# Kernel optimization log

Measured on AMD Instinct MI355X. Metric: run time of the kernel, lower is better.

The kernel has to match this reference:

```python
import jax, jax.numpy as jnp
import numpy as np

H = 768
NH = 12
HD = H // NH

def _layernorm(x, g, b, eps=1e-5):
    mu = jnp.mean(x, axis=-1, keepdims=True)
    var = jnp.var(x, axis=-1, keepdims=True)
    return (x - mu) * jax.lax.rsqrt(var + eps) * g + b

def setup_inputs() -> dict:
    key = jax.random.key(0)
    ks = jax.random.split(key, 16)
    s = 0.02
    inp = {
        "x": jax.random.normal(ks[0], (2, 2048, H), jnp.float32),
        "t": jax.random.normal(ks[1], (2, 1, H), jnp.float32),
        # MHA params
        "w_qkv": jax.random.normal(ks[2], (H, 3 * H), jnp.float32) * s,
        "b_qkv": jnp.zeros((3 * H,), jnp.float32),
        "w_mffn1": jax.random.normal(ks[3], (H, 4 * H), jnp.float32) * s,
        "b_mffn1": jnp.zeros((4 * H,), jnp.float32),
        "w_mffn2": jax.random.normal(ks[4], (4 * H, H), jnp.float32) * s,
        "b_mffn2": jnp.zeros((H,), jnp.float32),
        # scale_shift (adaLN) params
        "w_ss1": jax.random.normal(ks[5], (H, 6 * H), jnp.float32) * s,
        "b_ss1": jnp.zeros((6 * H,), jnp.float32),
        "w_ss2": jax.random.normal(ks[6], (6 * H, 6 * H), jnp.float32) * s,
        "b_ss2": jnp.zeros((6 * H,), jnp.float32),
        # layernorms
        "ln1_g": jnp.ones((H,), jnp.float32),
        "ln1_b": jnp.zeros((H,), jnp.float32),
        "ln2_g": jnp.ones((H,), jnp.float32),
        "ln2_b": jnp.zeros((H,), jnp.float32),
        # DiT block FFN
        "w_ffn1": jax.random.normal(ks[7], (H, 4 * H), jnp.float32) * s,
        "b_ffn1": jnp.zeros((4 * H,), jnp.float32),
        "w_ffn2": jax.random.normal(ks[8], (4 * H, H), jnp.float32) * s,
        "b_ffn2": jnp.zeros((H,), jnp.float32),
    }
    return inp

def _mha(x, w_qkv, b_qkv, w1, b1, w2, b2):
    B, T, _ = x.shape
    qkv = x @ w_qkv + b_qkv                      # [B,T,3H]
    qkv = qkv.reshape(B, T, 3, NH, HD)           # split (n h s) as in rearrange
    q, k, v = [jnp.transpose(qkv[:, :, i], (0, 2, 1, 3)) for i in range(3)]  # [B,NH,T,HD]
    # NOTE: faithful to source: scale by 1/sqrt(hidden_size), not head_dim
    wei = jnp.einsum('bhtd,bhsd->bhts', q, k) / jnp.sqrt(jnp.asarray(H, x.dtype))
    wei = jax.nn.softmax(wei, axis=-1)           # [B,NH,T,T] (dropout p=0)
    o = jnp.einsum('bhts,bhsd->bhtd', wei, v)    # [B,NH,T,HD]
    o = jnp.transpose(o, (0, 2, 1, 3)).reshape(B, T, H)
    o = jax.nn.gelu(o @ w1 + b1, approximate=False) @ w2 + b2
    return o

def reference(x, t, w_qkv, b_qkv, w_mffn1, b_mffn1, w_mffn2, b_mffn2,
              w_ss1, b_ss1, w_ss2, b_ss2, ln1_g, ln1_b, ln2_g, ln2_b,
              w_ffn1, b_ffn1, w_ffn2, b_ffn2):
    t_emb = jax.nn.silu(t @ w_ss1 + b_ss1) @ w_ss2 + b_ss2   # [B,1,6H]
    g1, be1, a1, g2, be2, a2 = jnp.split(t_emb, 6, axis=-1)  # each [B,1,H]
    residual = x
    h = g1 * _layernorm(x, ln1_g, ln1_b) + be1
    h = _mha(h, w_qkv, b_qkv, w_mffn1, b_mffn1, w_mffn2, b_mffn2)
    x = residual + a1 * h
    residual = x
    h = g2 * _layernorm(x, ln2_g, ln2_b) + be2
    h = jax.nn.gelu(h @ w_ffn1 + b_ffn1, approximate=False) @ w_ffn2 + b_ffn2
    x = residual + a2 * h
    return x
```

## Files before the change

### kernel.cpp

```cpp
#include <hip/hip_runtime.h>
#include <hip/hip_bf16.h>
#include <cstdint>

typedef __bf16 bf16x8 __attribute__((ext_vector_type(8)));
typedef float f32x4 __attribute__((ext_vector_type(4)));

#define SCALE_Q_LOG2E 0.052058770734702875f

__device__ inline float fast_exp2(float x) { return __builtin_amdgcn_exp2f(x); }

struct TransAll {
  const float* src[5];
  __hip_bfloat16* dst[5];
  int K[5], N[5];
  int start[6];
};

__global__ void k_transpose_all(TransAll ta) {
  __shared__ float tile[32][33];
  int bid = blockIdx.x;
  int i = 0;
#pragma unroll
  for (int j = 1; j < 5; ++j)
    if (bid >= ta.start[j]) i = j;
  int t0 = bid - ta.start[i];
  int N = ta.N[i], K = ta.K[i];
  int ntx = N >> 5;
  int bx = t0 % ntx, by = t0 / ntx;
  const float* src = ta.src[i];
  __hip_bfloat16* dst = ta.dst[i];
  int n0 = bx * 32, k0 = by * 32;
  int tx = threadIdx.x & 31, ty = threadIdx.x >> 5;
#pragma unroll
  for (int r = 0; r < 32; r += 8)
    tile[ty + r][tx] = src[(size_t)(k0 + ty + r) * N + n0 + tx];
  __syncthreads();
#pragma unroll
  for (int r = 0; r < 32; r += 8)
    dst[(size_t)(n0 + ty + r) * K + k0 + tx] = __float2bfloat16(tile[tx][ty + r]);
}

__global__ void k_tvec_gemm(const float* __restrict__ tin, const float* __restrict__ W,
                            float* __restrict__ acc_out, int K, int N, int KC) {
  int n = blockIdx.x * 256 + threadIdx.x;
  int kb = blockIdx.y * KC;
  float a0 = 0.f, a1 = 0.f;
  for (int k = kb; k < kb + KC; ++k) {
    float w = W[(size_t)k * N + n];
    a0 += tin[k] * w;
    a1 += tin[K + k] * w;
  }
  atomicAdd(&acc_out[n], a0);
  atomicAdd(&acc_out[N + n], a1);
}

__global__ void k_silu_bias(const float* __restrict__ acc, const float* __restrict__ bias,
                            float* __restrict__ out) {
  int i = blockIdx.x * 256 + threadIdx.x;
  int n = i; if (n >= 4608) n -= 4608;
  float v = acc[i] + bias[n];
  out[i] = v / (1.f + expf(-v));
}

__global__ void k_bias_add(const float* __restrict__ acc, const float* __restrict__ bias,
                           float* __restrict__ out) {
  int i = blockIdx.x * 256 + threadIdx.x;
  int n = i; if (n >= 4608) n -= 4608;
  out[i] = acc[i] + bias[n];
}

__global__ void k_ln_mod(const float* __restrict__ x, const float* __restrict__ lng,
                         const float* __restrict__ lnb, const float* __restrict__ temb,
                         int gofs, int bofs, __hip_bfloat16* __restrict__ out) {
  int row = blockIdx.x;
  int b = row >> 11;
  const float* xr = x + (size_t)row * 768;
  int tid = threadIdx.x;
  float v[3];
  float s = 0.f, sq = 0.f;
#pragma unroll
  for (int i = 0; i < 3; ++i) { v[i] = xr[tid + 256 * i]; s += v[i]; sq += v[i] * v[i]; }
#pragma unroll
  for (int o = 32; o > 0; o >>= 1) { s += __shfl_xor(s, o); sq += __shfl_xor(sq, o); }
  __shared__ float rs[4], rq[4];
  int w = tid >> 6, lane = tid & 63;
  if (lane == 0) { rs[w] = s; rq[w] = sq; }
  __syncthreads();
  s = rs[0] + rs[1] + rs[2] + rs[3];
  sq = rq[0] + rq[1] + rq[2] + rq[3];
  float mu = s * (1.f / 768.f);
  float var = sq * (1.f / 768.f) - mu * mu;
  float rstd = rsqrtf(var + 1e-5f);
  const float* tb = temb + (size_t)b * 4608;
#pragma unroll
  for (int i = 0; i < 3; ++i) {
    int n = tid + 256 * i;
    float h = (v[i] - mu) * rstd * lng[n] + lnb[n];
    h = tb[gofs + n] * h + tb[bofs + n];
    out[(size_t)row * 768 + n] = __float2bfloat16(h);
  }
}

template <int BM, int BN, int EPI>
__global__ __launch_bounds__(256)
void k_gemm(const __hip_bfloat16* __restrict__ A,
            const __hip_bfloat16* __restrict__ Bt,
            const float* __restrict__ bias,
            float* __restrict__ outF, __hip_bfloat16* __restrict__ outB,
            const float* __restrict__ res, const float* __restrict__ temb,
            int gofs, int M, int N, int K) {
  constexpr int MI = BM / 32;
  constexpr int NI = BN / 32;
  __shared__ __align__(16) __hip_bfloat16 As[BM * 64];
  __shared__ __align__(16) __hip_bfloat16 Bs[BN * 64];
  const int tid = threadIdx.x;
  const int w = tid >> 6, lane = tid & 63;
  const int quad = lane >> 4, l16 = lane & 15;
  const int wm = w & 1, wn = w >> 1;
  const int m0 = blockIdx.y * BM, n0 = blockIdx.x * BN;
  const int srow = lane >> 3;
  const int sco = ((lane & 7) ^ srow) * 8;

  f32x4 acc[MI][NI] = {};

  for (int k0 = 0; k0 < K; k0 += 64) {
#pragma unroll
    for (int ii = 0; ii < BM / 32; ++ii) {
      int is = w * (BM / 32) + ii;
      const __hip_bfloat16* g = A + (size_t)(m0 + is * 8 + srow) * K + k0 + sco;
      __builtin_amdgcn_global_load_lds(
          (const __attribute__((address_space(1))) void*)g,
          (__attribute__((address_space(3))) void*)&As[is * 512], 16, 0, 0);
    }
#pragma unroll
    for (int ii = 0; ii < BN / 32; ++ii) {
      int is = w * (BN / 32) + ii;
      const __hip_bfloat16* g = Bt + (size_t)(n0 + is * 8 + srow) * K + k0 + sco;
      __builtin_amdgcn_global_load_lds(
          (const __attribute__((address_space(1))) void*)g,
          (__attribute__((address_space(3))) void*)&Bs[is * 512], 16, 0, 0);
    }
    __syncthreads();
#pragma unroll
    for (int ks = 0; ks < 2; ++ks) {
      bf16x8 af[MI], bfv[NI];
#pragma unroll
      for (int i = 0; i < MI; ++i) {
        int row = wm * (BM / 2) + i * 16 + l16;
        int cph = (ks * 4 + quad) ^ (row & 7);
        af[i] = *(const bf16x8*)&As[row * 64 + cph * 8];
      }
#pragma unroll
      for (int j = 0; j < NI; ++j) {
        int row = wn * (BN / 2) + j * 16 + l16;
        int cph = (ks * 4 + quad) ^ (row & 7);
        bfv[j] = *(const bf16x8*)&Bs[row * 64 + cph * 8];
      }
#pragma unroll
      for (int i = 0; i < MI; ++i)
#pragma unroll
        for (int j = 0; j < NI; ++j)
          acc[i][j] = __builtin_amdgcn_mfma_f32_16x16x32_bf16(af[i], bfv[j], acc[i][j], 0, 0, 0);
    }
    __syncthreads();
  }

#pragma unroll
  for (int j = 0; j < NI; ++j) {
    int col = n0 + wn * (BN / 2) + j * 16 + l16;
    float bs = bias[col];
#pragma unroll
    for (int i = 0; i < MI; ++i) {
#pragma unroll
      for (int r = 0; r < 4; ++r) {
        int row = m0 + wm * (BM / 2) + i * 16 + quad * 4 + r;
        float v = acc[i][j][r] + bs;
        size_t idx = (size_t)row * N + col;
        if (EPI == 0) {
          outF[idx] = v;
        } else if (EPI == 1) {
          float v2 = v * v;
          float u = v * (0.79788456080286536f + 0.035677408136300125f * v2);
          float e = fast_exp2(u * 2.8853900817779268f);
          float gl = v - v * __builtin_amdgcn_rcpf(e + 1.f);
          outB[idx] = __float2bfloat16(gl);
        } else if (EPI == 2) {
          float gate = temb[(size_t)(row >> 11) * 4608 + gofs + col];
          outF[idx] = res[idx] + gate * v;
        } else {
          float vq = (col < 768) ? v * SCALE_Q_LOG2E : v;
          outB[idx] = __float2bfloat16(vq);
        }
      }
    }
  }
}

__global__ void k_prep_vt(const __hip_bfloat16* __restrict__ qkvb,
                          __hip_bfloat16* __restrict__ VT) {
  __shared__ float Vs[64][65];
  int st = blockIdx.x, bh = blockIdx.y;
  int b = bh / 12, nh = bh - b * 12;
  int tid = threadIdx.x;
  {
    int r = tid & 63, c0 = (tid >> 6) * 16;
    const __hip_bfloat16* src =
        qkvb + (size_t)(b * 2048 + st * 64 + r) * 2304 + 1536 + nh * 64 + c0;
    uint4 raw0 = *(const uint4*)src;
    uint4 raw1 = *(const uint4*)(src + 8);
    const __hip_bfloat16* e0 = (const __hip_bfloat16*)&raw0;
    const __hip_bfloat16* e1 = (const __hip_bfloat16*)&raw1;
#pragma unroll
    for (int j = 0; j < 8; ++j) Vs[r][c0 + j] = __bfloat162float(e0[j]);
#pragma unroll
    for (int j = 0; j < 8; ++j) Vs[r][c0 + 8 + j] = __bfloat162float(e1[j]);
  }
  __syncthreads();
  {
    int d = tid >> 2, s0 = (tid & 3) * 16;
    __hip_bfloat16 tmp[16];
#pragma unroll
    for (int j = 0; j < 16; ++j) tmp[j] = __float2bfloat16(Vs[s0 + j][d]);
    __hip_bfloat16* dst = VT + (size_t)(bh * 64 + d) * 2048 + st * 64 + s0;
    *(uint4*)dst = *(uint4*)&tmp[0];
    *(uint4*)(dst + 8) = *(uint4*)&tmp[8];
  }
}

__launch_bounds__(256)
__global__ void k_attn(const __hip_bfloat16* __restrict__ qkvb,
                       const __hip_bfloat16* __restrict__ VT,
                       __hip_bfloat16* __restrict__ out) {
  __shared__ __align__(16) __hip_bfloat16 Ks[128 * 64];
  __shared__ __align__(16) __hip_bfloat16 Vs[64 * 128];
  __shared__ __align__(16) __hip_bfloat16 Pw[4][16 * 128];

  const int tid = threadIdx.x;
  const int w = tid >> 6, lane = tid & 63;
  const int quad = lane >> 4, l16 = lane & 15;
  const int qt = blockIdx.x, nh = blockIdx.y, b = blockIdx.z;
  const int bh = b * 12 + nh;

  const int qrow0 = b * 2048 + qt * 64 + w * 16;
  bf16x8 qf[2];
#pragma unroll
  for (int t = 0; t < 2; ++t)
    qf[t] = *(const bf16x8*)(qkvb + (size_t)(qrow0 + l16) * 2304 + nh * 64 + t * 32 + quad * 8);

  bf16x8 ones;
#pragma unroll
  for (int j = 0; j < 8; ++j) ones[j] = (__bf16)1.0f;

  f32x4 o[4] = {};
  f32x4 o_l = {};

  const int srow8 = lane >> 3;
  const int sco8 = ((lane & 7) ^ srow8) * 8;
  const int srow4 = lane >> 4;

  for (int kt = 0; kt < 16; ++kt) {
    __syncthreads();
#pragma unroll
    for (int ii = 0; ii < 4; ++ii) {
      int i = w * 4 + ii;
      const __hip_bfloat16* gk =
          qkvb + (size_t)(b * 2048 + kt * 128 + i * 8 + srow8) * 2304 + 768 + nh * 64 + sco8;
      __builtin_amdgcn_global_load_lds(
          (const __attribute__((address_space(1))) void*)gk,
          (__attribute__((address_space(3))) void*)&Ks[i * 512], 16, 0, 0);
      int vrow = i * 4 + srow4;
      const __hip_bfloat16* gv =
          VT + (size_t)(bh * 64 + vrow) * 2048 + kt * 128 + (((lane & 15) ^ (vrow & 15)) * 8);
      __builtin_amdgcn_global_load_lds(
          (const __attribute__((address_space(1))) void*)gv,
          (__attribute__((address_space(3))) void*)&Vs[i * 512], 16, 0, 0);
    }
    __syncthreads();

    f32x4 s_acc[8] = {};
#pragma unroll
    for (int t = 0; t < 2; ++t) {
#pragma unroll
      for (int c = 0; c < 8; ++c) {
        int row = c * 16 + l16;
        int cph = (t * 4 + quad) ^ (row & 7);
        bf16x8 kf = *(const bf16x8*)&Ks[row * 64 + cph * 8];
        s_acc[c] = __builtin_amdgcn_mfma_f32_16x16x32_bf16(qf[t], kf, s_acc[c], 0, 0, 0);
      }
    }

#pragma unroll
    for (int c = 0; c < 8; ++c) {
      int chunk = c * 2 + (l16 >> 3);
#pragma unroll
      for (int r = 0; r < 4; ++r) {
        float p = fast_exp2(s_acc[c][r]);
        int row = quad * 4 + r;
        int phys = chunk ^ row;
        Pw[w][row * 128 + phys * 8 + (l16 & 7)] = __float2bfloat16(p);
      }
    }

#pragma unroll
    for (int t2 = 0; t2 < 4; ++t2) {
      int phys_p = ((t2 * 4 + quad) ^ l16);
      bf16x8 pa = *(const bf16x8*)&Pw[w][l16 * 128 + phys_p * 8];
#pragma unroll
      for (int nf = 0; nf < 4; ++nf) {
        int row = nf * 16 + l16;
        int cph = (t2 * 4 + quad) ^ (row & 15);
        bf16x8 vf = *(const bf16x8*)&Vs[row * 128 + cph * 8];
        o[nf] = __builtin_amdgcn_mfma_f32_16x16x32_bf16(pa, vf, o[nf], 0, 0, 0);
      }
      o_l = __builtin_amdgcn_mfma_f32_16x16x32_bf16(pa, ones, o_l, 0, 0, 0);
    }
  }

  {
    float inv[4];
#pragma unroll
    for (int r = 0; r < 4; ++r) inv[r] = 1.f / o_l[r];
#pragma unroll
    for (int nf = 0; nf < 4; ++nf)
#pragma unroll
      for (int r = 0; r < 4; ++r) {
        int row = qrow0 + quad * 4 + r;
        out[(size_t)row * 768 + nh * 64 + nf * 16 + l16] = __float2bfloat16(o[nf][r] * inv[r]);
      }
  }
}

extern "C" void kernel_launch(void* const* d_in, const int* in_sizes, int n_in,
                              void* d_out, int out_size, void* d_ws, size_t ws_size,
                              hipStream_t stream) {
  const float* x      = (const float*)d_in[0];
  const float* t      = (const float*)d_in[1];
  const float* w_qkv  = (const float*)d_in[2];
  const float* b_qkv  = (const float*)d_in[3];
  const float* w_m1   = (const float*)d_in[4];
  const float* b_m1   = (const float*)d_in[5];
  const float* w_m2   = (const float*)d_in[6];
  const float* b_m2   = (const float*)d_in[7];
  const float* w_ss1  = (const float*)d_in[8];
  const float* b_ss1  = (const float*)d_in[9];
  const float* w_ss2  = (const float*)d_in[10];
  const float* b_ss2  = (const float*)d_in[11];
  const float* ln1_g  = (const float*)d_in[12];
  const float* ln1_b  = (const float*)d_in[13];
  const float* ln2_g  = (const float*)d_in[14];
  const float* ln2_b  = (const float*)d_in[15];
  const float* w_f1   = (const float*)d_in[16];
  const float* b_f1   = (const float*)d_in[17];
  const float* w_f2   = (const float*)d_in[18];
  const float* b_f2   = (const float*)d_in[19];
  float* out = (float*)d_out;

  char* ws = (char*)d_ws;
  size_t off = 0;
  auto alloc = [&](size_t bytes) -> char* {
    off = (off + 255) & ~(size_t)255;
    char* p = ws + off;
    off += bytes;
    return p;
  };
  __hip_bfloat16* wtq  = (__hip_bfloat16*)alloc((size_t)2304 * 768 * 2);
  __hip_bfloat16* wtm1 = (__hip_bfloat16*)alloc((size_t)3072 * 768 * 2);
  __hip_bfloat16* wtm2 = (__hip_bfloat16*)alloc((size_t)768 * 3072 * 2);
  __hip_bfloat16* wtf1 = (__hip_bfloat16*)alloc((size_t)3072 * 768 * 2);
  __hip_bfloat16* wtf2 = (__hip_bfloat16*)alloc((size_t)768 * 3072 * 2);
  float* tacc1 = (float*)alloc(9216 * 4);
  float* tss   = (float*)alloc(9216 * 4);
  float* teacc = (float*)alloc(9216 * 4);
  float* temb  = (float*)alloc(9216 * 4);
  __hip_bfloat16* h1   = (__hip_bfloat16*)alloc((size_t)4096 * 768 * 2);
  __hip_bfloat16* qkvb = (__hip_bfloat16*)alloc((size_t)4096 * 2304 * 2);
  __hip_bfloat16* VT   = (__hip_bfloat16*)alloc((size_t)24 * 64 * 2048 * 2);
  __hip_bfloat16* attn = (__hip_bfloat16*)alloc((size_t)4096 * 768 * 2);
  __hip_bfloat16* act1 = (__hip_bfloat16*)alloc((size_t)4096 * 3072 * 2);
  float* x1            = (float*)alloc((size_t)4096 * 768 * 4);

  (void)hipMemsetAsync(tacc1, 0, 9216 * 4, stream);
  (void)hipMemsetAsync(teacc, 0, 9216 * 4, stream);

  TransAll ta;
  ta.src[0] = w_qkv; ta.dst[0] = wtq;  ta.K[0] = 768;  ta.N[0] = 2304;
  ta.src[1] = w_m1;  ta.dst[1] = wtm1; ta.K[1] = 768;  ta.N[1] = 3072;
  ta.src[2] = w_m2;  ta.dst[2] = wtm2; ta.K[2] = 3072; ta.N[2] = 768;
  ta.src[3] = w_f1;  ta.dst[3] = wtf1; ta.K[3] = 768;  ta.N[3] = 3072;
  ta.src[4] = w_f2;  ta.dst[4] = wtf2; ta.K[4] = 3072; ta.N[4] = 768;
  ta.start[0] = 0;
  ta.start[1] = ta.start[0] + (2304 / 32) * (768 / 32);
  ta.start[2] = ta.start[1] + (3072 / 32) * (768 / 32);
  ta.start[3] = ta.start[2] + (768 / 32) * (3072 / 32);
  ta.start[4] = ta.start[3] + (3072 / 32) * (768 / 32);
  ta.start[5] = ta.start[4] + (768 / 32) * (3072 / 32);
  k_transpose_all<<<ta.start[5], 256, 0, stream>>>(ta);

  k_tvec_gemm<<<dim3(4608 / 256, 768 / 64), 256, 0, stream>>>(t, w_ss1, tacc1, 768, 4608, 64);
  k_silu_bias<<<9216 / 256, 256, 0, stream>>>(tacc1, b_ss1, tss);
  k_tvec_gemm<<<dim3(4608 / 256, 4608 / 64), 256, 0, stream>>>(tss, w_ss2, teacc, 4608, 4608, 64);
  k_bias_add<<<9216 / 256, 256, 0, stream>>>(teacc, b_ss2, temb);

  k_ln_mod<<<4096, 256, 0, stream>>>(x, ln1_g, ln1_b, temb, 0, 768, h1);
  k_gemm<128, 128, 3><<<dim3(2304 / 128, 4096 / 128), 256, 0, stream>>>(
      h1, wtq, b_qkv, nullptr, qkvb, nullptr, nullptr, 0, 4096, 2304, 768);
  k_prep_vt<<<dim3(32, 24), 256, 0, stream>>>(qkvb, VT);
  k_attn<<<dim3(32, 12, 2), 256, 0, stream>>>(qkvb, VT, attn);
  k_gemm<128, 128, 1><<<dim3(3072 / 128, 4096 / 128), 256, 0, stream>>>(
      attn, wtm1, b_m1, nullptr, act1, nullptr, nullptr, 0, 4096, 3072, 768);
  k_gemm<64, 128, 2><<<dim3(768 / 128, 4096 / 64), 256, 0, stream>>>(
      act1, wtm2, b_m2, x1, nullptr, x, temb, 1536, 4096, 768, 3072);

  k_ln_mod<<<4096, 256, 0, stream>>>(x1, ln2_g, ln2_b, temb, 2304, 3072, h1);
  k_gemm<128, 128, 1><<<dim3(3072 / 128, 4096 / 128), 256, 0, stream>>>(
      h1, wtf1, b_f1, nullptr, act1, nullptr, nullptr, 0, 4096, 3072, 768);
  k_gemm<64, 128, 2><<<dim3(768 / 128, 4096 / 64), 256, 0, stream>>>(
      act1, wtf2, b_f2, out, nullptr, x1, temb, 3840, 4096, 768, 3072);
}
```

Before: 503.2 us.

## Fuse adaLN prep kernels, write V transpose from QKV GEMM, split attention keys across warps

Result: no change. 499.0 us (-0.8%).

```diff
diff --git a/kernel.cpp b/kernel.cpp
--- a/kernel.cpp
+++ b/kernel.cpp
@@ -9,68 +9,77 @@
 
 __device__ inline float fast_exp2(float x) { return __builtin_amdgcn_exp2f(x); }
 
-struct TransAll {
+struct PrepArgs {
   const float* src[5];
   __hip_bfloat16* dst[5];
   int K[5], N[5];
   int start[6];
+  const float* tin;
+  const float* w_ss1;
+  float* tacc1;
 };
 
-__global__ void k_transpose_all(TransAll ta) {
+__global__ void k_prep(PrepArgs pa) {
   __shared__ float tile[32][33];
   int bid = blockIdx.x;
-  int i = 0;
-#pragma unroll
-  for (int j = 1; j < 5; ++j)
-    if (bid >= ta.start[j]) i = j;
-  int t0 = bid - ta.start[i];
-  int N = ta.N[i], K = ta.K[i];
-  int ntx = N >> 5;
-  int bx = t0 % ntx, by = t0 / ntx;
-  const float* src = ta.src[i];
-  __hip_bfloat16* dst = ta.dst[i];
-  int n0 = bx * 32, k0 = by * 32;
-  int tx = threadIdx.x & 31, ty = threadIdx.x >> 5;
-#pragma unroll
-  for (int r = 0; r < 32; r += 8)
-    tile[ty + r][tx] = src[(size_t)(k0 + ty + r) * N + n0 + tx];
-  __syncthreads();
-#pragma unroll
-  for (int r = 0; r < 32; r += 8)
-    dst[(size_t)(n0 + ty + r) * K + k0 + tx] = __float2bfloat16(tile[tx][ty + r]);
-}
-
-__global__ void k_tvec_gemm(const float* __restrict__ tin, const float* __restrict__ W,
-                            float* __restrict__ acc_out, int K, int N, int KC) {
+  int tid = threadIdx.x;
+  if (bid < pa.start[5]) {
+    int i = 0;
+#pragma unroll
+    for (int j = 1; j < 5; ++j)
+      if (bid >= pa.start[j]) i = j;
+    int t0 = bid - pa.start[i];
+    int N = pa.N[i], K = pa.K[i];
+    int ntx = N >> 5;
+    int bx = t0 % ntx, by = t0 / ntx;
+    const float* src = pa.src[i];
+    __hip_bfloat16* dst = pa.dst[i];
+    int n0 = bx * 32, k0 = by * 32;
+    int tx = tid & 31, ty = tid >> 5;
+#pragma unroll
+    for (int r = 0; r < 32; r += 8)
+      tile[ty + r][tx] = src[(size_t)(k0 + ty + r) * N + n0 + tx];
+    __syncthreads();
+#pragma unroll
+    for (int r = 0; r < 32; r += 8)
+      dst[(size_t)(n0 + ty + r) * K + k0 + tx] = __float2bfloat16(tile[tx][ty + r]);
+  } else {
+    int t0 = bid - pa.start[5];
+    int nb = t0 % 18, kb0 = (t0 / 18) * 64;
+    int n = nb * 256 + tid;
+    float a0 = 0.f, a1 = 0.f;
+    for (int k = kb0; k < kb0 + 64; ++k) {
+      float w = pa.w_ss1[(size_t)k * 4608 + n];
+      a0 += pa.tin[k] * w;
+      a1 += pa.tin[768 + k] * w;
+    }
+    atomicAdd(&pa.tacc1[n], a0);
+    atomicAdd(&pa.tacc1[4608 + n], a1);
+  }
+}
+
+__global__ void k_tvec2_silu(const float* __restrict__ tacc1, const float* __restrict__ bss1,
+                             const float* __restrict__ W, float* __restrict__ teacc) {
   int n = blockIdx.x * 256 + threadIdx.x;
-  int kb = blockIdx.y * KC;
+  int kb = blockIdx.y * 64;
   float a0 = 0.f, a1 = 0.f;
-  for (int k = kb; k < kb + KC; ++k) {
-    float w = W[(size_t)k * N + n];
-    a0 += tin[k] * w;
-    a1 += tin[K + k] * w;
-  }
-  atomicAdd(&acc_out[n], a0);
-  atomicAdd(&acc_out[N + n], a1);
-}
-
-__global__ void k_silu_bias(const float* __restrict__ acc, const float* __restrict__ bias,
-                            float* __restrict__ out) {
-  int i = blockIdx.x * 256 + threadIdx.x;
-  int n = i; if (n >= 4608) n -= 4608;
-  float v = acc[i] + bias[n];
-  out[i] = v / (1.f + expf(-v));
-}
-
-__global__ void k_bias_add(const float* __restrict__ acc, const float* __restrict__ bias,
-                           float* __restrict__ out) {
-  int i = blockIdx.x * 256 + threadIdx.x;
-  int n = i; if (n >= 4608) n -= 4608;
-  out[i] = acc[i] + bias[n];
+  for (int k = kb; k < kb + 64; ++k) {
+    float w = W[(size_t)k * 4608 + n];
+    float bs = bss1[k];
+    float t0 = tacc1[k] + bs;
+    float t1 = tacc1[4608 + k] + bs;
+    t0 = t0 / (1.f + expf(-t0));
+    t1 = t1 / (1.f + expf(-t1));
+    a0 += t0 * w;
+    a1 += t1 * w;
+  }
+  atomicAdd(&teacc[n], a0);
+  atomicAdd(&teacc[4608 + n], a1);
 }
 
 __global__ void k_ln_mod(const float* __restrict__ x, const float* __restrict__ lng,
-                         const float* __restrict__ lnb, const float* __restrict__ temb,
+                         const float* __restrict__ lnb, const float* __restrict__ teacc,
+                         const float* __restrict__ bss2,
                          int gofs, int bofs, __hip_bfloat16* __restrict__ out) {
   int row = blockIdx.x;
   int b = row >> 11;
@@ -91,12 +100,14 @@
   float mu = s * (1.f / 768.f);
   float var = sq * (1.f / 768.f) - mu * mu;
   float rstd = rsqrtf(var + 1e-5f);
-  const float* tb = temb + (size_t)b * 4608;
+  const float* tb = teacc + (size_t)b * 4608;
 #pragma unroll
   for (int i = 0; i < 3; ++i) {
     int n = tid + 256 * i;
+    float gv = tb[gofs + n] + bss2[gofs + n];
+    float bv = tb[bofs + n] + bss2[bofs + n];
     float h = (v[i] - mu) * rstd * lng[n] + lnb[n];
-    h = tb[gofs + n] * h + tb[bofs + n];
+    h = gv * h + bv;
     out[(size_t)row * 768 + n] = __float2bfloat16(h);
   }
 }
@@ -107,7 +118,9 @@
             const __hip_bfloat16* __restrict__ Bt,
             const float* __restrict__ bias,
             float* __restrict__ outF, __hip_bfloat16* __restrict__ outB,
-            const float* __restrict__ res, const float* __restrict__ temb,
+            __hip_bfloat16* __restrict__ outV,
+            const float* __restrict__ res, const float* __restrict__ teacc,
+            const float* __restrict__ bss2,
             int gofs, int M, int N, int K) {
   constexpr int MI = BM / 32;
   constexpr int NI = BN / 32;
@@ -171,59 +184,39 @@
     float bs = bias[col];
 #pragma unroll
     for (int i = 0; i < MI; ++i) {
-#pragma unroll
-      for (int r = 0; r < 4; ++r) {
-        int row = m0 + wm * (BM / 2) + i * 16 + quad * 4 + r;
-        float v = acc[i][j][r] + bs;
-        size_t idx = (size_t)row * N + col;
-        if (EPI == 0) {
-          outF[idx] = v;
-        } else if (EPI == 1) {
-          float v2 = v * v;
-          float u = v * (0.79788456080286536f + 0.035677408136300125f * v2);
-          float e = fast_exp2(u * 2.8853900817779268f);
-          float gl = v - v * __builtin_amdgcn_rcpf(e + 1.f);
-          outB[idx] = __float2bfloat16(gl);
-        } else if (EPI == 2) {
-          float gate = temb[(size_t)(row >> 11) * 4608 + gofs + col];
-          outF[idx] = res[idx] + gate * v;
-        } else {
-          float vq = (col < 768) ? v * SCALE_Q_LOG2E : v;
-          outB[idx] = __float2bfloat16(vq);
+      int row0 = m0 + wm * (BM / 2) + i * 16 + quad * 4;
+      if (EPI == 3 && col >= 1536) {
+        int d = col - 1536;
+        int nh = d >> 6, dl = d & 63;
+        int bb = row0 >> 11, tok = row0 & 2047;
+        __hip_bfloat16 tmp[4];
+#pragma unroll
+        for (int r = 0; r < 4; ++r) tmp[r] = __float2bfloat16(acc[i][j][r] + bs);
+        *(uint2*)&outV[((size_t)(bb * 12 + nh) * 64 + dl) * 2048 + tok] = *(uint2*)tmp;
+      } else {
+#pragma unroll
+        for (int r = 0; r < 4; ++r) {
+          int row = row0 + r;
+          float v = acc[i][j][r] + bs;
+          size_t idx = (size_t)row * N + col;
+          if (EPI == 0) {
+            outF[idx] = v;
+          } else if (EPI == 1) {
+            float v2 = v * v;
+            float u = v * (0.79788456080286536f + 0.035677408136300125f * v2);
+            float e = fast_exp2(u * 2.8853900817779268f);
+            float gl = v - v * __builtin_amdgcn_rcpf(e + 1.f);
+            outB[idx] = __float2bfloat16(gl);
+          } else if (EPI == 2) {
+            float gate = teacc[(size_t)(row >> 11) * 4608 + gofs + col] + bss2[gofs + col];
+            outF[idx] = res[idx] + gate * v;
+          } else {
+            float vq = (col < 768) ? v * SCALE_Q_LOG2E : v;
+            outB[idx] = __float2bfloat16(vq);
+          }
         }
       }
     }
-  }
-}
-
-__global__ void k_prep_vt(const __hip_bfloat16* __restrict__ qkvb,
-                          __hip_bfloat16* __restrict__ VT) {
-  __shared__ float Vs[64][65];
-  int st = blockIdx.x, bh = blockIdx.y;
-  int b = bh / 12, nh = bh - b * 12;
-  int tid = threadIdx.x;
-  {
-    int r = tid & 63, c0 = (tid >> 6) * 16;
-    const __hip_bfloat16* src =
-        qkvb + (size_t)(b * 2048 + st * 64 + r) * 2304 + 1536 + nh * 64 + c0;
-    uint4 raw0 = *(const uint4*)src;
-    uint4 raw1 = *(const uint4*)(src + 8);
-    const __hip_bfloat16* e0 = (const __hip_bfloat16*)&raw0;
-    const __hip_bfloat16* e1 = (const __hip_bfloat16*)&raw1;
-#pragma unroll
-    for (int j = 0; j < 8; ++j) Vs[r][c0 + j] = __bfloat162float(e0[j]);
-#pragma unroll
-    for (int j = 0; j < 8; ++j) Vs[r][c0 + 8 + j] = __bfloat162float(e1[j]);
-  }
-  __syncthreads();
-  {
-    int d = tid >> 2, s0 = (tid & 3) * 16;
-    __hip_bfloat16 tmp[16];
-#pragma unroll
-    for (int j = 0; j < 16; ++j) tmp[j] = __float2bfloat16(Vs[s0 + j][d]);
-    __hip_bfloat16* dst = VT + (size_t)(bh * 64 + d) * 2048 + st * 64 + s0;
-    *(uint4*)dst = *(uint4*)&tmp[0];
-    *(uint4*)(dst + 8) = *(uint4*)&tmp[8];
   }
 }
 
@@ -233,26 +226,30 @@
                        __hip_bfloat16* __restrict__ out) {
   __shared__ __align__(16) __hip_bfloat16 Ks[128 * 64];
   __shared__ __align__(16) __hip_bfloat16 Vs[64 * 128];
-  __shared__ __align__(16) __hip_bfloat16 Pw[4][16 * 128];
+  __shared__ __align__(16) __hip_bfloat16 Pw[4][32 * 64];
 
   const int tid = threadIdx.x;
   const int w = tid >> 6, lane = tid & 63;
   const int quad = lane >> 4, l16 = lane & 15;
+  const int wm = w & 1, wn = w >> 1;
   const int qt = blockIdx.x, nh = blockIdx.y, b = blockIdx.z;
   const int bh = b * 12 + nh;
 
-  const int qrow0 = b * 2048 + qt * 64 + w * 16;
-  bf16x8 qf[2];
-#pragma unroll
-  for (int t = 0; t < 2; ++t)
-    qf[t] = *(const bf16x8*)(qkvb + (size_t)(qrow0 + l16) * 2304 + nh * 64 + t * 32 + quad * 8);
+  const int qrow0 = b * 2048 + qt * 64 + wm * 32;
+  bf16x8 qf[2][2];
+#pragma unroll
+  for (int mi = 0; mi < 2; ++mi)
+#pragma unroll
+    for (int t = 0; t < 2; ++t)
+      qf[mi][t] = *(const bf16x8*)(qkvb + (size_t)(qrow0 + mi * 16 + l16) * 2304 +
+                                   nh * 64 + t * 32 + quad * 8);
 
   bf16x8 ones;
 #pragma unroll
   for (int j = 0; j < 8; ++j) ones[j] = (__bf16)1.0f;
 
-  f32x4 o[4] = {};
-  f32x4 o_l = {};
+  f32x4 o[2][4] = {};
+  f32x4 o_l[2] = {};
 
   const int srow8 = lane >> 3;
   const int sco8 = ((lane & 7) ^ srow8) * 8;
@@ -277,56 +274,98 @@
     }
     __syncthreads();
 
-    f32x4 s_acc[8] = {};
+    f32x4 s_acc[2][4] = {};
 #pragma unroll
     for (int t = 0; t < 2; ++t) {
-#pragma unroll
-      for (int c = 0; c < 8; ++c) {
-        int row = c * 16 + l16;
+      bf16x8 kf[4];
+#pragma unroll
+      for (int c = 0; c < 4; ++c) {
+        int row = wn * 64 + c * 16 + l16;
         int cph = (t * 4 + quad) ^ (row & 7);
-        bf16x8 kf = *(const bf16x8*)&Ks[row * 64 + cph * 8];
-        s_acc[c] = __builtin_amdgcn_mfma_f32_16x16x32_bf16(qf[t], kf, s_acc[c], 0, 0, 0);
-      }
-    }
-
-#pragma unroll
-    for (int c = 0; c < 8; ++c) {
-      int chunk = c * 2 + (l16 >> 3);
-#pragma unroll
-      for (int r = 0; r < 4; ++r) {
-        float p = fast_exp2(s_acc[c][r]);
-        int row = quad * 4 + r;
-        int phys = chunk ^ row;
-        Pw[w][row * 128 + phys * 8 + (l16 & 7)] = __float2bfloat16(p);
-      }
-    }
-
-#pragma unroll
-    for (int t2 = 0; t2 < 4; ++t2) {
-      int phys_p = ((t2 * 4 + quad) ^ l16);
-      bf16x8 pa = *(const bf16x8*)&Pw[w][l16 * 128 + phys_p * 8];
+        kf[c] = *(const bf16x8*)&Ks[row * 64 + cph * 8];
+      }
+#pragma unroll
+      for (int mi = 0; mi < 2; ++mi)
+#pragma unroll
+        for (int c = 0; c < 4; ++c)
+          s_acc[mi][c] = __builtin_amdgcn_mfma_f32_16x16x32_bf16(qf[mi][t], kf[c], s_acc[mi][c], 0, 0, 0);
+    }
+
+#pragma unroll
+    for (int mi = 0; mi < 2; ++mi)
+#pragma unroll
+      for (int c = 0; c < 4; ++c) {
+        int chunk = c * 2 + (l16 >> 3);
+#pragma unroll
+        for (int r = 0; r < 4; ++r) {
+          float p = fast_exp2(s_acc[mi][c][r]);
+          int row = mi * 16 + quad * 4 + r;
+          int phys = chunk ^ (row & 7);
+          Pw[w][row * 64 + phys * 8 + (l16 & 7)] = __float2bfloat16(p);
+        }
+      }
+
+#pragma unroll
+    for (int t2 = 0; t2 < 2; ++t2) {
+      bf16x8 pa[2];
+#pragma unroll
+      for (int mi = 0; mi < 2; ++mi) {
+        int row = mi * 16 + l16;
+        int phys = (t2 * 4 + quad) ^ (row & 7);
+        pa[mi] = *(const bf16x8*)&Pw[w][row * 64 + phys * 8];
+      }
+      bf16x8 vf[4];
 #pragma unroll
       for (int nf = 0; nf < 4; ++nf) {
         int row = nf * 16 + l16;
-        int cph = (t2 * 4 + quad) ^ (row & 15);
-        bf16x8 vf = *(const bf16x8*)&Vs[row * 128 + cph * 8];
-        o[nf] = __builtin_amdgcn_mfma_f32_16x16x32_bf16(pa, vf, o[nf], 0, 0, 0);
-      }
-      o_l = __builtin_amdgcn_mfma_f32_16x16x32_bf16(pa, ones, o_l, 0, 0, 0);
-    }
-  }
-
-  {
-    float inv[4];
-#pragma unroll
-    for (int r = 0; r < 4; ++r) inv[r] = 1.f / o_l[r];
-#pragma unroll
-    for (int nf = 0; nf < 4; ++nf)
+        int cph = (wn * 8 + t2 * 4 + quad) ^ (row & 15);
+        vf[nf] = *(const bf16x8*)&Vs[row * 128 + cph * 8];
+      }
+#pragma unroll
+      for (int mi = 0; mi < 2; ++mi) {
+#pragma unroll
+        for (int nf = 0; nf < 4; ++nf)
+          o[mi][nf] = __builtin_amdgcn_mfma_f32_16x16x32_bf16(pa[mi], vf[nf], o[mi][nf], 0, 0, 0);
+        o_l[mi] = __builtin_amdgcn_mfma_f32_16x16x32_bf16(pa[mi], ones, o_l[mi], 0, 0, 0);
+      }
+    }
+  }
+
+  __syncthreads();
+  float* Cb = (float*)Ks;
+  float* Lb = (float*)Vs;
+  if (wn == 1) {
+#pragma unroll
+    for (int mi = 0; mi < 2; ++mi) {
+#pragma unroll
+      for (int nf = 0; nf < 4; ++nf)
+#pragma unroll
+        for (int r = 0; r < 4; ++r)
+          Cb[((wm * 32 + mi * 16 + quad * 4 + r)) * 64 + nf * 16 + l16] = o[mi][nf][r];
+      if (l16 == 0)
+#pragma unroll
+        for (int r = 0; r < 4; ++r) Lb[wm * 32 + mi * 16 + quad * 4 + r] = o_l[mi][r];
+    }
+  }
+  __syncthreads();
+  if (wn == 0) {
+#pragma unroll
+    for (int mi = 0; mi < 2; ++mi) {
+      float inv[4];
 #pragma unroll
       for (int r = 0; r < 4; ++r) {
-        int row = qrow0 + quad * 4 + r;
-        out[(size_t)row * 768 + nh * 64 + nf * 16 + l16] = __float2bfloat16(o[nf][r] * inv[r]);
-      }
+        float lt = o_l[mi][r] + Lb[wm * 32 + mi * 16 + quad * 4 + r];
+        inv[r] = 1.f / lt;
+      }
+#pragma unroll
+      for (int nf = 0; nf < 4; ++nf)
+#pragma unroll
+        for (int r = 0; r < 4; ++r) {
+          float ov = o[mi][nf][r] + Cb[(wm * 32 + mi * 16 + quad * 4 + r) * 64 + nf * 16 + l16];
+          int row = qrow0 + mi * 16 + quad * 4 + r;
+          out[(size_t)row * 768 + nh * 64 + nf * 16 + l16] = __float2bfloat16(ov * inv[r]);
+        }
+    }
   }
 }
 
@@ -369,9 +408,7 @@
   __hip_bfloat16* wtf1 = (__hip_bfloat16*)alloc((size_t)3072 * 768 * 2);
   __hip_bfloat16* wtf2 = (__hip_bfloat16*)alloc((size_t)768 * 3072 * 2);
   float* tacc1 = (float*)alloc(9216 * 4);
-  float* tss   = (float*)alloc(9216 * 4);
   float* teacc = (float*)alloc(9216 * 4);
-  float* temb  = (float*)alloc(9216 * 4);
   __hip_bfloat16* h1   = (__hip_bfloat16*)alloc((size_t)4096 * 768 * 2);
   __hip_bfloat16* qkvb = (__hip_bfloat16*)alloc((size_t)4096 * 2304 * 2);
   __hip_bfloat16* VT   = (__hip_bfloat16*)alloc((size_t)24 * 64 * 2048 * 2);
@@ -382,38 +419,36 @@
   (void)hipMemsetAsync(tacc1, 0, 9216 * 4, stream);
   (void)hipMemsetAsync(teacc, 0, 9216 * 4, stream);
 
-  TransAll ta;
-  ta.src[0] = w_qkv; ta.dst[0] = wtq;  ta.K[0] = 768;  ta.N[0] = 2304;
-  ta.src[1] = w_m1;  ta.dst[1] = wtm1; ta.K[1] = 768;  ta.N[1] = 3072;
-  ta.src[2] = w_m2;  ta.dst[2] = wtm2; ta.K[2] = 3072; ta.N[2] = 768;
-  ta.src[3] = w_f1;  ta.dst[3] = wtf1; ta.K[3] = 768;  ta.N[3] = 3072;
-  ta.src[4] = w_f2;  ta.dst[4] = wtf2; ta.K[4] = 3072; ta.N[4] = 768;
-  ta.start[0] = 0;
-  ta.start[1] = ta.start[0] + (2304 / 32) * (768 / 32);
-  ta.start[2] = ta.start[1] + (3072 / 32) * (768 / 32);
-  ta.start[3] = ta.start[2] + (768 / 32) * (3072 / 32);
-  ta.start[4] = ta.start[3] + (3072 / 32) * (768 / 32);
-  ta.start[5] = ta.start[4] + (768 / 32) * (3072 / 32);
-  k_transpose_all<<<ta.start[5], 256, 0, stream>>>(ta);
-
-  k_tvec_gemm<<<dim3(4608 / 256, 768 / 64), 256, 0, stream>>>(t, w_ss1, tacc1, 768, 4608, 64);
-  k_silu_bias<<<9216 / 256, 256, 0, stream>>>(tacc1, b_ss1, tss);
-  k_tvec_gemm<<<dim3(4608 / 256, 4608 / 64), 256, 0, stream>>>(tss, w_ss2, teacc, 4608, 4608, 64);
-  k_bias_add<<<9216 / 256, 256, 0, stream>>>(teacc, b_ss2, temb);
-
-  k_ln_mod<<<4096, 256, 0, stream>>>(x, ln1_g, ln1_b, temb, 0, 768, h1);
-  k_gemm<128, 128, 3><<<dim3(2304 / 128, 4096 / 128), 256, 0, stream>>>(
-      h1, wtq, b_qkv, nullptr, qkvb, nullptr, nullptr, 0, 4096, 2304, 768);
-  k_prep_vt<<<dim3(32, 24), 256, 0, stream>>>(qkvb, VT);
+  PrepArgs pa;
+  pa.src[0] = w_qkv; pa.dst[0] = wtq;  pa.K[0] = 768;  pa.N[0] = 2304;
+  pa.src[1] = w_m1;  pa.dst[1] = wtm1; pa.K[1] = 768;  pa.N[1] = 3072;
+  pa.src[2] = w_m2;  pa.dst[2] = wtm2; pa.K[2] = 3072; pa.N[2] = 768;
+  pa.src[3] = w_f1;  pa.dst[3] = wtf1; pa.K[3] = 768;  pa.N[3] = 3072;
+  pa.src[4] = w_f2;  pa.dst[4] = wtf2; pa.K[4] = 3072; pa.N[4] = 768;
+  pa.start[0] = 0;
+  pa.start[1] = pa.start[0] + (2304 / 32) * (768 / 32);
+  pa.start[2] = pa.start[1] + (3072 / 32) * (768 / 32);
+  pa.start[3] = pa.start[2] + (768 / 32) * (3072 / 32);
+  pa.start[4] = pa.start[3] + (3072 / 32) * (768 / 32);
+  pa.start[5] = pa.start[4] + (768 / 32) * (3072 / 32);
+  pa.tin = t; pa.w_ss1 = w_ss1; pa.tacc1 = tacc1;
+  int tvec1_blocks = 18 * 12;
+  k_prep<<<pa.start[5] + tvec1_blocks, 256, 0, stream>>>(pa);
+
+  k_tvec2_silu<<<dim3(4608 / 256, 4608 / 64), 256, 0, stream>>>(tacc1, b_ss1, w_ss2, teacc);
+
+  k_ln_mod<<<4096, 256, 0, stream>>>(x, ln1_g, ln1_b, teacc, b_ss2, 0, 768, h1);
+  k_gemm<64, 128, 3><<<dim3(2304 / 128, 4096 / 64), 256, 0, stream>>>(
+      h1, wtq, b_qkv, nullptr, qkvb, VT, nullptr, nullptr, nullptr, 0, 4096, 2304, 768);
   k_attn<<<dim3(32, 12, 2), 256, 0, stream>>>(qkvb, VT, attn);
   k_gemm<128, 128, 1><<<dim3(3072 / 128, 4096 / 128), 256, 0, stream>>>(
-      attn, wtm1, b_m1, nullptr, act1, nullptr, nullptr, 0, 4096, 3072, 768);
+      attn, wtm1, b_m1, nullptr, act1, nullptr, nullptr, nullptr, nullptr, 0, 4096, 3072, 768);
   k_gemm<64, 128, 2><<<dim3(768 / 128, 4096 / 64), 256, 0, stream>>>(
-      act1, wtm2, b_m2, x1, nullptr, x, temb, 1536, 4096, 768, 3072);
-
-  k_ln_mod<<<4096, 256, 0, stream>>>(x1, ln2_g, ln2_b, temb, 2304, 3072, h1);
+      act1, wtm2, b_m2, x1, nullptr, nullptr, x, teacc, b_ss2, 1536, 4096, 768, 3072);
+
+  k_ln_mod<<<4096, 256, 0, stream>>>(x1, ln2_g, ln2_b, teacc, b_ss2, 2304, 3072, h1);
   k_gemm<128, 128, 1><<<dim3(3072 / 128, 4096 / 128), 256, 0, stream>>>(
-      h1, wtf1, b_f1, nullptr, act1, nullptr, nullptr, 0, 4096, 3072, 768);
+      h1, wtf1, b_f1, nullptr, act1, nullptr, nullptr, nullptr, nullptr, 0, 4096, 3072, 768);
   k_gemm<64, 128, 2><<<dim3(768 / 128, 4096 / 64), 256, 0, stream>>>(
-      act1, wtf2, b_f2, out, nullptr, x1, temb, 3840, 4096, 768, 3072);
-}
+      act1, wtf2, b_f2, out, nullptr, nullptr, x1, teacc, b_ss2, 3840, 4096, 768, 3072);
+}
```
